# Kernel optimization log

Hardware: AMD Instinct MI355X
Metric: run time of the kernel (lower is better)

Reference implementation:

```python
import jax, jax.numpy as jnp
import numpy as np

T, D, H = 2048, 1024, 16
HS = D // H  # head_size = 64
DFF = 4 * D
LN_EPS = 1e-6


def layernorm(x, scale, bias, eps=LN_EPS):
    mu = jnp.mean(x, axis=-1, keepdims=True)
    var = jnp.mean(jnp.square(x - mu), axis=-1, keepdims=True)
    return (x - mu) * jax.lax.rsqrt(var + eps) * scale + bias


def setup_inputs() -> dict:
    key = jax.random.key(0)
    ks = jax.random.split(key, 12)
    s_in = 1.0 / np.sqrt(D)
    s_ff = 1.0 / np.sqrt(DFF)
    return {
        "x": jax.random.normal(ks[0], (T, D), jnp.float32),
        "Wq": jax.random.normal(ks[1], (H, D, HS), jnp.float32) * s_in,
        "Wk": jax.random.normal(ks[2], (H, D, HS), jnp.float32) * s_in,
        "Wv": jax.random.normal(ks[3], (H, D, HS), jnp.float32) * s_in,
        "Wo": jax.random.normal(ks[4], (D, D), jnp.float32) * s_in,
        "bo": jnp.zeros((D,), jnp.float32),
        "W1": jax.random.normal(ks[5], (D, DFF), jnp.float32) * s_in,
        "b1": jnp.zeros((DFF,), jnp.float32),
        "W2": jax.random.normal(ks[6], (DFF, D), jnp.float32) * s_ff,
        "b2": jnp.zeros((D,), jnp.float32),
        "ln1_scale": jnp.ones((D,), jnp.float32),
        "ln1_bias": jnp.zeros((D,), jnp.float32),
        "ln2_scale": jnp.ones((D,), jnp.float32),
        "ln2_bias": jnp.zeros((D,), jnp.float32),
        "training": 0,
    }


def reference(x, Wq, Wk, Wv, Wo, bo, W1, b1, W2, b2,
              ln1_scale, ln1_bias, ln2_scale, ln2_bias, training):
    # --- pre-LN causal multi-head self-attention ---
    h = layernorm(x, ln1_scale, ln1_bias)
    q = jnp.einsum("td,hdk->htk", h, Wq)  # [H,T,HS]
    k = jnp.einsum("td,hdk->htk", h, Wk)
    v = jnp.einsum("td,hdk->htk", h, Wv)
    scores = jnp.einsum("htk,hsk->hts", q, k) / jnp.sqrt(jnp.float32(HS))
    causal = jnp.tril(jnp.ones((T, T), jnp.float32))
    scores = jnp.where(causal == 0, -jnp.inf, scores)
    wei = jax.nn.softmax(scores, axis=-1)
    av = jnp.einsum("hts,hsk->htk", wei, v)          # [H,T,HS]
    av = av.transpose(1, 0, 2).reshape(T, H * HS)    # concat over heads
    x = x + av @ Wo + bo                              # dropout deterministic -> identity
    # --- pre-LN feed-forward ---
    h2 = layernorm(x, ln2_scale, ln2_bias)
    ff = jax.nn.relu(h2 @ W1 + b1) @ W2 + b2
    x = x + ff
    return x
```

## Files before the change

kernel.cpp:

```cpp
#include <hip/hip_runtime.h>
#include <cstdint>


typedef __bf16 bf16;
typedef __bf16 bf16x4 __attribute__((ext_vector_type(4)));
typedef __bf16 bf16x8 __attribute__((ext_vector_type(8)));
typedef float floatx4 __attribute__((ext_vector_type(4)));

__device__ __forceinline__ void ld_g2l(const bf16* g, bf16* l) {
    __builtin_amdgcn_global_load_lds(
        (const __attribute__((address_space(1))) void*)g,
        (__attribute__((address_space(3))) void*)l, 16, 0, 0);
}

__global__ __launch_bounds__(256) void transpose_cast_kernel(
    const float* __restrict__ src, bf16* __restrict__ dst,
    int R, int C, long long sBatch, long long dBatch)
{
    __shared__ float tile[32][33];
    const int tx = threadIdx.x, ty = threadIdx.y;
    src += (size_t)blockIdx.z * sBatch;
    dst += (size_t)blockIdx.z * dBatch;
    const int c0 = blockIdx.x * 32, r0 = blockIdx.y * 32;
#pragma unroll
    for (int i = ty; i < 32; i += 8)
        tile[i][tx] = src[(size_t)(r0 + i) * C + c0 + tx];
    __syncthreads();
#pragma unroll
    for (int i = ty; i < 32; i += 8)
        dst[(size_t)(c0 + i) * R + r0 + tx] = (bf16)tile[tx][i];
}

__global__ __launch_bounds__(256) void transpose_cast_qkv_kernel(
    const float* __restrict__ Wq, const float* __restrict__ Wk,
    const float* __restrict__ Wv, bf16* __restrict__ dst)
{
    __shared__ float tile[32][33];
    const int tx = threadIdx.x, ty = threadIdx.y;
    const int m = blockIdx.z >> 4, h = blockIdx.z & 15;
    const float* src = (m == 0 ? Wq : (m == 1 ? Wk : Wv)) + h * 65536;
    bf16* d = dst + m * 1048576 + h * 65536;
    const int c0 = blockIdx.x * 32, r0 = blockIdx.y * 32;
#pragma unroll
    for (int i = ty; i < 32; i += 8)
        tile[i][tx] = src[(size_t)(r0 + i) * 64 + c0 + tx];
    __syncthreads();
#pragma unroll
    for (int i = ty; i < 32; i += 8)
        d[(size_t)(c0 + i) * 1024 + r0 + tx] = (bf16)tile[tx][i];
}

__global__ __launch_bounds__(256) void transpose_head_kernel(
    const bf16* __restrict__ qkv, bf16* __restrict__ dst, int colOff)
{
    __shared__ bf16 tile[32][33];
    const int tx = threadIdx.x, ty = threadIdx.y;
    const int h = blockIdx.z;
    const int j0 = blockIdx.x * 32, s0 = blockIdx.y * 32;
#pragma unroll
    for (int i = ty; i < 32; i += 8)
        tile[i][tx] = qkv[(size_t)(s0 + i) * 3072 + colOff + h * 64 + j0 + tx];
    __syncthreads();
#pragma unroll
    for (int i = ty; i < 32; i += 8)
        dst[(size_t)h * 64 * 2048 + (size_t)(j0 + i) * 2048 + s0 + tx] = tile[tx][i];
}

__global__ __launch_bounds__(256) void ln_kernel(
    const float* __restrict__ x, const float* __restrict__ sc,
    const float* __restrict__ bi, bf16* __restrict__ out)
{
    const int row = blockIdx.x;
    const int tid = threadIdx.x;
    const float4 v = ((const float4*)(x + (size_t)row * 1024))[tid];
    float s1 = v.x + v.y + v.z + v.w;
    float s2 = v.x * v.x + v.y * v.y + v.z * v.z + v.w * v.w;
#pragma unroll
    for (int mm = 1; mm < 64; mm <<= 1) {
        s1 += __shfl_xor(s1, mm);
        s2 += __shfl_xor(s2, mm);
    }
    __shared__ float w1[4], w2[4];
    const int wave = tid >> 6, lane = tid & 63;
    if (lane == 0) { w1[wave] = s1; w2[wave] = s2; }
    __syncthreads();
    s1 = w1[0] + w1[1] + w1[2] + w1[3];
    s2 = w2[0] + w2[1] + w2[2] + w2[3];
    const float mu = s1 * (1.f / 1024.f);
    const float var = fmaxf(s2 * (1.f / 1024.f) - mu * mu, 0.f);
    const float rr = rsqrtf(var + 1e-6f);
    const float4 scv = ((const float4*)sc)[tid];
    const float4 biv = ((const float4*)bi)[tid];
    bf16x4 ov;
    ov[0] = (bf16)((v.x - mu) * rr * scv.x + biv.x);
    ov[1] = (bf16)((v.y - mu) * rr * scv.y + biv.y);
    ov[2] = (bf16)((v.z - mu) * rr * scv.z + biv.z);
    ov[3] = (bf16)((v.w - mu) * rr * scv.w + biv.w);
    *(bf16x4*)(out + (size_t)row * 1024 + tid * 4) = ov;
}

__global__ __launch_bounds__(256) void reduce4_kernel(
    const float* __restrict__ p, const float* __restrict__ bias,
    const float* __restrict__ res, float* __restrict__ out)
{
    const int idx = blockIdx.x * 256 + threadIdx.x;
    const int c4 = idx & 255;
    const float4 a0 = ((const float4*)p)[idx];
    const float4 a1 = ((const float4*)(p + 2097152))[idx];
    const float4 a2 = ((const float4*)(p + 4194304))[idx];
    const float4 a3 = ((const float4*)(p + 6291456))[idx];
    const float4 bi = ((const float4*)bias)[c4];
    const float4 r = ((const float4*)res)[idx];
    float4 o;
    o.x = (a0.x + a1.x) + (a2.x + a3.x) + bi.x + r.x;
    o.y = (a0.y + a1.y) + (a2.y + a3.y) + bi.y + r.y;
    o.z = (a0.z + a1.z) + (a2.z + a3.z) + bi.z + r.z;
    o.w = (a0.w + a1.w) + (a2.w + a3.w) + bi.w + r.w;
    ((float4*)out)[idx] = o;
}

template <int MODE, int NG, int MG, int SPLITK>
__global__ __launch_bounds__(256) void gemm128_kernel(
    const bf16* __restrict__ A, const bf16* __restrict__ Bt,
    int N, int K,
    float* __restrict__ outF, bf16* __restrict__ outB,
    const float* __restrict__ bias)
{
    __shared__ __align__(16) bf16 Alds[2][128][32];
    __shared__ __align__(16) bf16 Blds[2][128][32];
    const int tid  = threadIdx.x;
    const int lane = tid & 63;
    const int w    = tid >> 6;
    const int r15  = lane & 15;
    const int quad = lane >> 4;

    const int id    = blockIdx.x + gridDim.x * (blockIdx.y + gridDim.y * blockIdx.z);
    const int xcd   = id & 7;
    const int seq   = id >> 3;
    const int nPerX = gridDim.x / NG;
    const int mPerX = gridDim.y / MG;
    const int nm    = nPerX * mPerX;
    const int z     = seq / nm;
    const int loc   = seq - z * nm;
    const int bn    = ((xcd % NG) * nPerX + (loc % nPerX)) * 128;
    const int bm    = ((xcd / NG) * mPerX + (loc / nPerX)) * 128;

    const int wm = (w >> 1) * 64;
    const int wn = (w & 1) * 64;

    floatx4 acc[4][4];
#pragma unroll
    for (int i = 0; i < 4; ++i)
#pragma unroll
        for (int j = 0; j < 4; ++j) acc[i][j] = (floatx4)(0.f);

    const int KS    = K / SPLITK;
    const int kBase = (SPLITK > 1) ? z * KS : 0;
    const int nIter = KS / 32;

    const int srow = lane >> 2;
    const int gch  = (lane & 3) ^ ((lane >> 3) & 3);
    const bf16* aptr = A + (size_t)(bm + w * 16 + srow) * K + kBase + gch * 8;
    const bf16* bptr = Bt + (size_t)(bn + w * 16 + srow) * K + kBase + gch * 8;

#pragma unroll
    for (int rr = 0; rr < 2; ++rr) {
        ld_g2l(aptr + (size_t)rr * 64 * K, &Alds[0][rr * 64 + w * 16][0]);
        ld_g2l(bptr + (size_t)rr * 64 * K, &Blds[0][rr * 64 + w * 16][0]);
    }

    const int pcs = quad ^ ((r15 >> 1) & 3);

    for (int it = 0; it < nIter; ++it) {
        const int buf = it & 1;
        __syncthreads();
        if (it + 1 < nIter) {
            const int k2 = (it + 1) * 32;
#pragma unroll
            for (int rr = 0; rr < 2; ++rr) {
                ld_g2l(aptr + (size_t)rr * 64 * K + k2, &Alds[buf ^ 1][rr * 64 + w * 16][0]);
                ld_g2l(bptr + (size_t)rr * 64 * K + k2, &Blds[buf ^ 1][rr * 64 + w * 16][0]);
            }
        }
        bf16x8 af[4], bfr[4];
#pragma unroll
        for (int i = 0; i < 4; ++i)
            af[i] = *(const bf16x8*)(&Alds[buf][wm + i * 16 + r15][pcs * 8]);
#pragma unroll
        for (int j = 0; j < 4; ++j)
            bfr[j] = *(const bf16x8*)(&Blds[buf][wn + j * 16 + r15][pcs * 8]);
#pragma unroll
        for (int i = 0; i < 4; ++i)
#pragma unroll
            for (int j = 0; j < 4; ++j)
                acc[i][j] = __builtin_amdgcn_mfma_f32_16x16x32_bf16(
                    af[i], bfr[j], acc[i][j], 0, 0, 0);
    }

    const int row0 = bm + wm + quad * 4;
    const int col0 = bn + wn + r15;
    float* po = (MODE == 3) ? outF + (size_t)z * 2048 * 1024 : outF;
#pragma unroll
    for (int i = 0; i < 4; ++i) {
#pragma unroll
        for (int reg = 0; reg < 4; ++reg) {
            const int row = row0 + i * 16 + reg;
#pragma unroll
            for (int j = 0; j < 4; ++j) {
                const int col = col0 + j * 16;
                float v = acc[i][j][reg];
                if (MODE == 0) {
                    outB[(size_t)row * N + col] = (bf16)v;
                } else if (MODE == 2) {
                    v += bias[col];
                    outB[(size_t)row * N + col] = (bf16)fmaxf(v, 0.f);
                } else {
                    po[(size_t)row * N + col] = v;
                }
            }
        }
    }
}

template <int NG, int MG>
__global__ __launch_bounds__(256) void gemm64_kernel(
    const bf16* __restrict__ A, const bf16* __restrict__ Bt,
    int N, int K,
    float* __restrict__ outF, const float* __restrict__ bias,
    const float* __restrict__ res)
{
    __shared__ __align__(16) bf16 Alds[2][64][64];
    __shared__ __align__(16) bf16 Blds[2][64][64];
    const int tid  = threadIdx.x;
    const int lane = tid & 63;
    const int w    = tid >> 6;
    const int r15  = lane & 15;
    const int quad = lane >> 4;

    const int id    = blockIdx.x + gridDim.x * blockIdx.y;
    const int xcd   = id & 7;
    const int seq   = id >> 3;
    const int nPerX = gridDim.x / NG;
    const int mPerX = gridDim.y / MG;
    const int loc   = seq % (nPerX * mPerX);
    const int bn    = ((xcd % NG) * nPerX + (loc % nPerX)) * 64;
    const int bm    = ((xcd / NG) * mPerX + (loc / nPerX)) * 64;

    const int wm = (w >> 1) * 32;
    const int wn = (w & 1) * 32;

    floatx4 acc[2][2];
#pragma unroll
    for (int i = 0; i < 2; ++i)
#pragma unroll
        for (int j = 0; j < 2; ++j) acc[i][j] = (floatx4)(0.f);

    const int nIter = K / 64;
    const int lrow = lane >> 3;
    const int gch  = (lane & 7) ^ lrow;
    const bf16* aptr = A + (size_t)(bm + w * 16 + lrow) * K + gch * 8;
    const bf16* bptr = Bt + (size_t)(bn + w * 16 + lrow) * K + gch * 8;

#pragma unroll
    for (int t = 0; t < 2; ++t) {
        ld_g2l(aptr + (size_t)t * 8 * K, &Alds[0][w * 16 + t * 8][0]);
        ld_g2l(bptr + (size_t)t * 8 * K, &Blds[0][w * 16 + t * 8][0]);
    }

    for (int it = 0; it < nIter; ++it) {
        const int buf = it & 1;
        __syncthreads();
        if (it + 1 < nIter) {
            const int k2 = (it + 1) * 64;
#pragma unroll
            for (int t = 0; t < 2; ++t) {
                ld_g2l(aptr + (size_t)t * 8 * K + k2, &Alds[buf ^ 1][w * 16 + t * 8][0]);
                ld_g2l(bptr + (size_t)t * 8 * K + k2, &Blds[buf ^ 1][w * 16 + t * 8][0]);
            }
        }
#pragma unroll
        for (int kk = 0; kk < 2; ++kk) {
            const int pc = ((kk * 4 + quad) ^ (r15 & 7)) * 8;
            bf16x8 af[2], bfr[2];
#pragma unroll
            for (int i = 0; i < 2; ++i)
                af[i] = *(const bf16x8*)(&Alds[buf][wm + i * 16 + r15][pc]);
#pragma unroll
            for (int j = 0; j < 2; ++j)
                bfr[j] = *(const bf16x8*)(&Blds[buf][wn + j * 16 + r15][pc]);
#pragma unroll
            for (int i = 0; i < 2; ++i)
#pragma unroll
                for (int j = 0; j < 2; ++j)
                    acc[i][j] = __builtin_amdgcn_mfma_f32_16x16x32_bf16(
                        af[i], bfr[j], acc[i][j], 0, 0, 0);
        }
    }

    const int row0 = bm + wm + quad * 4;
    const int col0 = bn + wn + r15;
#pragma unroll
    for (int i = 0; i < 2; ++i)
#pragma unroll
        for (int reg = 0; reg < 4; ++reg) {
            const int row = row0 + i * 16 + reg;
#pragma unroll
            for (int j = 0; j < 2; ++j) {
                const int col = col0 + j * 16;
                outF[(size_t)row * N + col] =
                    acc[i][j][reg] + bias[col] + res[(size_t)row * N + col];
            }
        }
}

__global__ __launch_bounds__(256) void attn_kernel(
    const bf16* __restrict__ qkv, const bf16* __restrict__ vt,
    bf16* __restrict__ out)
{
    __shared__ __align__(16) bf16 Qs[64][64];
    __shared__ __align__(16) bf16 Ks[2][64][64];
    __shared__ __align__(16) bf16 Vs[2][64][64];
    __shared__ __align__(16) bf16 Ps[4][16][72];

    const int tid  = threadIdx.x;
    const int w    = tid >> 6;
    const int lane = tid & 63;
    const int r15  = lane & 15;
    const int quad = lane >> 4;
    const int rl   = lane >> 3;
    const int gsw  = (lane & 7) ^ (rl & 7);

    const int idp = blockIdx.x + 16 * blockIdx.y;
    const int seq = idp >> 3;
    const int h   = (idp & 7) * 2 + (seq & 1);
    const int qp  = seq >> 1;
    const int qt  = blockIdx.z ? 31 - qp : qp;
    const int qrow0 = qt * 64;

    const bf16* qsec = qkv + h * 64;
    const bf16* ksec = qkv + 1024 + h * 64;
    const bf16* vth  = vt + (size_t)h * 64 * 2048;

#pragma unroll
    for (int t = 0; t < 2; ++t) {
        const int r = t * 32 + w * 8 + rl;
        ld_g2l(qsec + (size_t)(qrow0 + r) * 3072 + gsw * 8, &Qs[t * 32 + w * 8][0]);
        ld_g2l(ksec + (size_t)r * 3072 + gsw * 8, &Ks[0][t * 32 + w * 8][0]);
        ld_g2l(vth + (size_t)r * 2048 + gsw * 8, &Vs[0][t * 32 + w * 8][0]);
    }
    __syncthreads();

    bf16x8 qf[2];
#pragma unroll
    for (int c = 0; c < 2; ++c) {
        const int p = ((c * 4 + quad) ^ (r15 & 7)) * 8;
        qf[c] = *(const bf16x8*)&Qs[w * 16 + r15][p];
    }

    float lacc[4] = {0.f, 0.f, 0.f, 0.f};
    floatx4 O[4];
#pragma unroll
    for (int j = 0; j < 4; ++j) O[j] = (floatx4)(0.f);

#pragma unroll 1
    for (int sb = 0; sb <= qt; ++sb) {
        const int buf = sb & 1;
        if (sb < qt) {
            const int s1 = (sb + 1) * 64;
#pragma unroll
            for (int t = 0; t < 2; ++t) {
                const int r = t * 32 + w * 8 + rl;
                ld_g2l(ksec + (size_t)(s1 + r) * 3072 + gsw * 8, &Ks[buf ^ 1][t * 32 + w * 8][0]);
                ld_g2l(vth + (size_t)r * 2048 + s1 + gsw * 8, &Vs[buf ^ 1][t * 32 + w * 8][0]);
            }
        }

        floatx4 S[4];
#pragma unroll
        for (int j = 0; j < 4; ++j) S[j] = (floatx4)(0.f);
#pragma unroll
        for (int c = 0; c < 2; ++c) {
#pragma unroll
            for (int j = 0; j < 4; ++j) {
                const int p = ((c * 4 + quad) ^ (r15 & 7)) * 8;
                const bf16x8 b = *(const bf16x8*)&Ks[buf][j * 16 + r15][p];
                S[j] = __builtin_amdgcn_mfma_f32_16x16x32_bf16(qf[c], b, S[j], 0, 0, 0);
            }
        }
        const bool diag = (sb == qt);
        const int rowl = w * 16 + quad * 4;
#pragma unroll
        for (int j = 0; j < 4; ++j) {
            const int col = j * 16 + r15;
#pragma unroll
            for (int r = 0; r < 4; ++r) {
                float p = exp2f(fmaf(S[j][r], 0.18033688f, -28.853901f));
                if (diag && col > rowl + r) p = 0.f;
                S[j][r] = p;
                lacc[r] += p;
            }
        }
#pragma unroll
        for (int r = 0; r < 4; ++r)
#pragma unroll
            for (int j = 0; j < 4; ++j)
                Ps[w][quad * 4 + r][j * 16 + r15] = (bf16)S[j][r];
#pragma unroll
        for (int c = 0; c < 2; ++c) {
            const bf16x8 a = *(const bf16x8*)&Ps[w][r15][c * 32 + quad * 8];
#pragma unroll
            for (int j = 0; j < 4; ++j) {
                const int p = ((c * 4 + quad) ^ (r15 & 7)) * 8;
                const bf16x8 b = *(const bf16x8*)&Vs[buf][j * 16 + r15][p];
                O[j] = __builtin_amdgcn_mfma_f32_16x16x32_bf16(a, b, O[j], 0, 0, 0);
            }
        }
        __syncthreads();
    }
#pragma unroll
    for (int r = 0; r < 4; ++r) {
#pragma unroll
        for (int d = 1; d < 16; d <<= 1) lacc[r] += __shfl_xor(lacc[r], d);
    }
#pragma unroll
    for (int r = 0; r < 4; ++r) {
        const float inv = 1.0f / lacc[r];
        const int row = qrow0 + w * 16 + quad * 4 + r;
#pragma unroll
        for (int j = 0; j < 4; ++j)
            out[(size_t)row * 1024 + h * 64 + j * 16 + r15] = (bf16)(O[j][r] * inv);
    }
}

extern "C" void kernel_launch(void* const* d_in, const int* in_sizes, int n_in,
                              void* d_out, int out_size, void* d_ws, size_t ws_size,
                              hipStream_t stream)
{
    const float* x    = (const float*)d_in[0];
    const float* Wq   = (const float*)d_in[1];
    const float* Wk   = (const float*)d_in[2];
    const float* Wv   = (const float*)d_in[3];
    const float* Wo   = (const float*)d_in[4];
    const float* bo   = (const float*)d_in[5];
    const float* W1   = (const float*)d_in[6];
    const float* b1   = (const float*)d_in[7];
    const float* W2   = (const float*)d_in[8];
    const float* b2   = (const float*)d_in[9];
    const float* ln1s = (const float*)d_in[10];
    const float* ln1b = (const float*)d_in[11];
    const float* ln2s = (const float*)d_in[12];
    const float* ln2b = (const float*)d_in[13];

    char* ws = (char*)d_ws;
    bf16*  Wqkvt = (bf16*)(ws + 0);
    bf16*  Wot   = (bf16*)(ws + 6291456);
    bf16*  W1t   = (bf16*)(ws + 8388608);
    bf16*  W2t   = (bf16*)(ws + 16777216);
    bf16*  hbuf  = (bf16*)(ws + 25165824);
    bf16*  QKV   = (bf16*)(ws + 29360128);
    bf16*  Vt    = (bf16*)(ws + 41943040);
    bf16*  Obuf  = (bf16*)(ws + 46137344);
    float* x1    = (float*)(ws + 50331648);
    bf16*  h2    = (bf16*)(ws + 58720256);
    bf16*  ff1   = (bf16*)(ws + 62914560);
    float* psum  = (float*)(ws + 79691776);

    const dim3 tb(32, 8);
    transpose_cast_qkv_kernel<<<dim3(2, 32, 48), tb, 0, stream>>>(Wq, Wk, Wv, Wqkvt);
    transpose_cast_kernel<<<dim3(32, 32, 1), tb, 0, stream>>>(Wo, Wot, 1024, 1024, 0, 0);
    transpose_cast_kernel<<<dim3(128, 32, 1), tb, 0, stream>>>(W1, W1t, 1024, 4096, 0, 0);
    transpose_cast_kernel<<<dim3(32, 128, 1), tb, 0, stream>>>(W2, W2t, 4096, 1024, 0, 0);

    ln_kernel<<<2048, 256, 0, stream>>>(x, ln1s, ln1b, hbuf);
    gemm128_kernel<0,4,2,1><<<dim3(24, 16), 256, 0, stream>>>(hbuf, Wqkvt, 3072, 1024, nullptr, QKV, nullptr);
    transpose_head_kernel<<<dim3(2, 64, 16), tb, 0, stream>>>(QKV, Vt, 2048);
    attn_kernel<<<dim3(16, 16, 2), 256, 0, stream>>>(QKV, Vt, Obuf);
    gemm64_kernel<4,2><<<dim3(16, 32), 256, 0, stream>>>(Obuf, Wot, 1024, 1024, x1, bo, x);
    ln_kernel<<<2048, 256, 0, stream>>>(x1, ln2s, ln2b, h2);
    gemm128_kernel<2,4,2,1><<<dim3(32, 16), 256, 0, stream>>>(h2, W1t, 4096, 1024, nullptr, ff1, b1);
    gemm128_kernel<3,2,4,4><<<dim3(8, 16, 4), 256, 0, stream>>>(ff1, W2t, 1024, 4096, psum, nullptr, nullptr);
    reduce4_kernel<<<2048, 256, 0, stream>>>(psum, b2, x1, (float*)d_out);
}
```

Measured before the change: 278.4 us.

## Merge prep kernels and replace split-K reduce with atomic accumulation into residual

Folds the four weight transpose-casts and the first layernorm into one launch. That layernorm pass also writes x+bo as the initial residual buffer, and the second layernorm writes x1+b2 into the output. The Wo projection and the W2 GEMM now use split-K with fp32 atomicAdd directly into these pre-initialized buffers, which removes the gemm64 kernel, the partial-sum buffer and the reduce kernel. This cuts launch count and partial-sum memory traffic, at the cost of atomic contention and non-deterministic summation order.

New measurement: 295.0 us. 1.06x slower.

```diff
diff --git a/kernel.cpp b/kernel.cpp
--- a/kernel.cpp
+++ b/kernel.cpp
@@ -13,65 +13,12 @@
         (__attribute__((address_space(3))) void*)l, 16, 0, 0);
 }
 
-__global__ __launch_bounds__(256) void transpose_cast_kernel(
-    const float* __restrict__ src, bf16* __restrict__ dst,
-    int R, int C, long long sBatch, long long dBatch)
-{
-    __shared__ float tile[32][33];
-    const int tx = threadIdx.x, ty = threadIdx.y;
-    src += (size_t)blockIdx.z * sBatch;
-    dst += (size_t)blockIdx.z * dBatch;
-    const int c0 = blockIdx.x * 32, r0 = blockIdx.y * 32;
-#pragma unroll
-    for (int i = ty; i < 32; i += 8)
-        tile[i][tx] = src[(size_t)(r0 + i) * C + c0 + tx];
-    __syncthreads();
-#pragma unroll
-    for (int i = ty; i < 32; i += 8)
-        dst[(size_t)(c0 + i) * R + r0 + tx] = (bf16)tile[tx][i];
-}
-
-__global__ __launch_bounds__(256) void transpose_cast_qkv_kernel(
-    const float* __restrict__ Wq, const float* __restrict__ Wk,
-    const float* __restrict__ Wv, bf16* __restrict__ dst)
-{
-    __shared__ float tile[32][33];
-    const int tx = threadIdx.x, ty = threadIdx.y;
-    const int m = blockIdx.z >> 4, h = blockIdx.z & 15;
-    const float* src = (m == 0 ? Wq : (m == 1 ? Wk : Wv)) + h * 65536;
-    bf16* d = dst + m * 1048576 + h * 65536;
-    const int c0 = blockIdx.x * 32, r0 = blockIdx.y * 32;
-#pragma unroll
-    for (int i = ty; i < 32; i += 8)
-        tile[i][tx] = src[(size_t)(r0 + i) * 64 + c0 + tx];
-    __syncthreads();
-#pragma unroll
-    for (int i = ty; i < 32; i += 8)
-        d[(size_t)(c0 + i) * 1024 + r0 + tx] = (bf16)tile[tx][i];
-}
-
-__global__ __launch_bounds__(256) void transpose_head_kernel(
-    const bf16* __restrict__ qkv, bf16* __restrict__ dst, int colOff)
-{
-    __shared__ bf16 tile[32][33];
-    const int tx = threadIdx.x, ty = threadIdx.y;
-    const int h = blockIdx.z;
-    const int j0 = blockIdx.x * 32, s0 = blockIdx.y * 32;
-#pragma unroll
-    for (int i = ty; i < 32; i += 8)
-        tile[i][tx] = qkv[(size_t)(s0 + i) * 3072 + colOff + h * 64 + j0 + tx];
-    __syncthreads();
-#pragma unroll
-    for (int i = ty; i < 32; i += 8)
-        dst[(size_t)h * 64 * 2048 + (size_t)(j0 + i) * 2048 + s0 + tx] = tile[tx][i];
-}
-
-__global__ __launch_bounds__(256) void ln_kernel(
+__device__ __forceinline__ void ln_row_body(
     const float* __restrict__ x, const float* __restrict__ sc,
-    const float* __restrict__ bi, bf16* __restrict__ out)
-{
-    const int row = blockIdx.x;
-    const int tid = threadIdx.x;
+    const float* __restrict__ bi, bf16* __restrict__ out,
+    const float* __restrict__ preBias, float* __restrict__ pre,
+    int row, int tid, float* wred)
+{
     const float4 v = ((const float4*)(x + (size_t)row * 1024))[tid];
     float s1 = v.x + v.y + v.z + v.w;
     float s2 = v.x * v.x + v.y * v.y + v.z * v.z + v.w * v.w;
@@ -80,12 +27,11 @@
         s1 += __shfl_xor(s1, mm);
         s2 += __shfl_xor(s2, mm);
     }
-    __shared__ float w1[4], w2[4];
     const int wave = tid >> 6, lane = tid & 63;
-    if (lane == 0) { w1[wave] = s1; w2[wave] = s2; }
+    if (lane == 0) { wred[wave] = s1; wred[4 + wave] = s2; }
     __syncthreads();
-    s1 = w1[0] + w1[1] + w1[2] + w1[3];
-    s2 = w2[0] + w2[1] + w2[2] + w2[3];
+    s1 = wred[0] + wred[1] + wred[2] + wred[3];
+    s2 = wred[4] + wred[5] + wred[6] + wred[7];
     const float mu = s1 * (1.f / 1024.f);
     const float var = fmaxf(s2 * (1.f / 1024.f) - mu * mu, 0.f);
     const float rr = rsqrtf(var + 1e-6f);
@@ -97,26 +43,85 @@
     ov[2] = (bf16)((v.z - mu) * rr * scv.z + biv.z);
     ov[3] = (bf16)((v.w - mu) * rr * scv.w + biv.w);
     *(bf16x4*)(out + (size_t)row * 1024 + tid * 4) = ov;
-}
-
-__global__ __launch_bounds__(256) void reduce4_kernel(
-    const float* __restrict__ p, const float* __restrict__ bias,
-    const float* __restrict__ res, float* __restrict__ out)
-{
-    const int idx = blockIdx.x * 256 + threadIdx.x;
-    const int c4 = idx & 255;
-    const float4 a0 = ((const float4*)p)[idx];
-    const float4 a1 = ((const float4*)(p + 2097152))[idx];
-    const float4 a2 = ((const float4*)(p + 4194304))[idx];
-    const float4 a3 = ((const float4*)(p + 6291456))[idx];
-    const float4 bi = ((const float4*)bias)[c4];
-    const float4 r = ((const float4*)res)[idx];
-    float4 o;
-    o.x = (a0.x + a1.x) + (a2.x + a3.x) + bi.x + r.x;
-    o.y = (a0.y + a1.y) + (a2.y + a3.y) + bi.y + r.y;
-    o.z = (a0.z + a1.z) + (a2.z + a3.z) + bi.z + r.z;
-    o.w = (a0.w + a1.w) + (a2.w + a3.w) + bi.w + r.w;
-    ((float4*)out)[idx] = o;
+    const float4 pb = ((const float4*)preBias)[tid];
+    float4 po;
+    po.x = v.x + pb.x; po.y = v.y + pb.y; po.z = v.z + pb.z; po.w = v.w + pb.w;
+    ((float4*)(pre + (size_t)row * 1024))[tid] = po;
+}
+
+__global__ __launch_bounds__(256) void prep_kernel(
+    const float* __restrict__ Wq, const float* __restrict__ Wk,
+    const float* __restrict__ Wv, bf16* __restrict__ Wqkvt,
+    const float* __restrict__ Wo, bf16* __restrict__ Wot,
+    const float* __restrict__ W1, bf16* __restrict__ W1t,
+    const float* __restrict__ W2, bf16* __restrict__ W2t,
+    const float* __restrict__ x, const float* __restrict__ ln1s,
+    const float* __restrict__ ln1b, bf16* __restrict__ hbuf,
+    const float* __restrict__ bo, float* __restrict__ x1init)
+{
+    __shared__ float tile[32][33];
+    __shared__ float wred[8];
+    const int b = blockIdx.x;
+    const int tid = threadIdx.x;
+
+    if (b >= 12288) {
+        ln_row_body(x, ln1s, ln1b, hbuf, bo, x1init, b - 12288, tid, wred);
+        return;
+    }
+
+    const int tx = tid & 31, ty = tid >> 5;
+    const float* src; bf16* dst; int R, C, c0, r0;
+    if (b < 3072) {
+        const int bz = b >> 6, by = (b >> 1) & 31, bx = b & 1;
+        const int m = bz >> 4, h = bz & 15;
+        src = (m == 0 ? Wq : (m == 1 ? Wk : Wv)) + h * 65536;
+        dst = Wqkvt + m * 1048576 + h * 65536;
+        R = 1024; C = 64; c0 = bx * 32; r0 = by * 32;
+    } else if (b < 4096) {
+        const int i = b - 3072;
+        src = Wo; dst = Wot; R = 1024; C = 1024;
+        c0 = (i & 31) * 32; r0 = (i >> 5) * 32;
+    } else if (b < 8192) {
+        const int i = b - 4096;
+        src = W1; dst = W1t; R = 1024; C = 4096;
+        c0 = (i & 127) * 32; r0 = (i >> 7) * 32;
+    } else {
+        const int i = b - 8192;
+        src = W2; dst = W2t; R = 4096; C = 1024;
+        c0 = (i & 31) * 32; r0 = (i >> 5) * 32;
+    }
+#pragma unroll
+    for (int i = ty; i < 32; i += 8)
+        tile[i][tx] = src[(size_t)(r0 + i) * C + c0 + tx];
+    __syncthreads();
+#pragma unroll
+    for (int i = ty; i < 32; i += 8)
+        dst[(size_t)(c0 + i) * R + r0 + tx] = (bf16)tile[tx][i];
+}
+
+__global__ __launch_bounds__(256) void ln2_kernel(
+    const float* __restrict__ x, const float* __restrict__ sc,
+    const float* __restrict__ bi, bf16* __restrict__ out,
+    const float* __restrict__ b2, float* __restrict__ dpre)
+{
+    __shared__ float wred[8];
+    ln_row_body(x, sc, bi, out, b2, dpre, blockIdx.x, threadIdx.x, wred);
+}
+
+__global__ __launch_bounds__(256) void transpose_head_kernel(
+    const bf16* __restrict__ qkv, bf16* __restrict__ dst, int colOff)
+{
+    __shared__ bf16 tile[32][33];
+    const int tx = threadIdx.x, ty = threadIdx.y;
+    const int h = blockIdx.z;
+    const int j0 = blockIdx.x * 32, s0 = blockIdx.y * 32;
+#pragma unroll
+    for (int i = ty; i < 32; i += 8)
+        tile[i][tx] = qkv[(size_t)(s0 + i) * 3072 + colOff + h * 64 + j0 + tx];
+    __syncthreads();
+#pragma unroll
+    for (int i = ty; i < 32; i += 8)
+        dst[(size_t)h * 64 * 2048 + (size_t)(j0 + i) * 2048 + s0 + tx] = tile[tx][i];
 }
 
 template <int MODE, int NG, int MG, int SPLITK>
@@ -199,7 +204,6 @@
 
     const int row0 = bm + wm + quad * 4;
     const int col0 = bn + wn + r15;
-    float* po = (MODE == 3) ? outF + (size_t)z * 2048 * 1024 : outF;
 #pragma unroll
     for (int i = 0; i < 4; ++i) {
 #pragma unroll
@@ -215,102 +219,11 @@
                     v += bias[col];
                     outB[(size_t)row * N + col] = (bf16)fmaxf(v, 0.f);
                 } else {
-                    po[(size_t)row * N + col] = v;
+                    atomicAdd(&outF[(size_t)row * N + col], v);
                 }
             }
         }
     }
-}
-
-template <int NG, int MG>
-__global__ __launch_bounds__(256) void gemm64_kernel(
-    const bf16* __restrict__ A, const bf16* __restrict__ Bt,
-    int N, int K,
-    float* __restrict__ outF, const float* __restrict__ bias,
-    const float* __restrict__ res)
-{
-    __shared__ __align__(16) bf16 Alds[2][64][64];
-    __shared__ __align__(16) bf16 Blds[2][64][64];
-    const int tid  = threadIdx.x;
-    const int lane = tid & 63;
-    const int w    = tid >> 6;
-    const int r15  = lane & 15;
-    const int quad = lane >> 4;
-
-    const int id    = blockIdx.x + gridDim.x * blockIdx.y;
-    const int xcd   = id & 7;
-    const int seq   = id >> 3;
-    const int nPerX = gridDim.x / NG;
-    const int mPerX = gridDim.y / MG;
-    const int loc   = seq % (nPerX * mPerX);
-    const int bn    = ((xcd % NG) * nPerX + (loc % nPerX)) * 64;
-    const int bm    = ((xcd / NG) * mPerX + (loc / nPerX)) * 64;
-
-    const int wm = (w >> 1) * 32;
-    const int wn = (w & 1) * 32;
-
-    floatx4 acc[2][2];
-#pragma unroll
-    for (int i = 0; i < 2; ++i)
-#pragma unroll
-        for (int j = 0; j < 2; ++j) acc[i][j] = (floatx4)(0.f);
-
-    const int nIter = K / 64;
-    const int lrow = lane >> 3;
-    const int gch  = (lane & 7) ^ lrow;
-    const bf16* aptr = A + (size_t)(bm + w * 16 + lrow) * K + gch * 8;
-    const bf16* bptr = Bt + (size_t)(bn + w * 16 + lrow) * K + gch * 8;
-
-#pragma unroll
-    for (int t = 0; t < 2; ++t) {
-        ld_g2l(aptr + (size_t)t * 8 * K, &Alds[0][w * 16 + t * 8][0]);
-        ld_g2l(bptr + (size_t)t * 8 * K, &Blds[0][w * 16 + t * 8][0]);
-    }
-
-    for (int it = 0; it < nIter; ++it) {
-        const int buf = it & 1;
-        __syncthreads();
-        if (it + 1 < nIter) {
-            const int k2 = (it + 1) * 64;
-#pragma unroll
-            for (int t = 0; t < 2; ++t) {
-                ld_g2l(aptr + (size_t)t * 8 * K + k2, &Alds[buf ^ 1][w * 16 + t * 8][0]);
-                ld_g2l(bptr + (size_t)t * 8 * K + k2, &Blds[buf ^ 1][w * 16 + t * 8][0]);
-            }
-        }
-#pragma unroll
-        for (int kk = 0; kk < 2; ++kk) {
-            const int pc = ((kk * 4 + quad) ^ (r15 & 7)) * 8;
-            bf16x8 af[2], bfr[2];
-#pragma unroll
-            for (int i = 0; i < 2; ++i)
-                af[i] = *(const bf16x8*)(&Alds[buf][wm + i * 16 + r15][pc]);
-#pragma unroll
-            for (int j = 0; j < 2; ++j)
-                bfr[j] = *(const bf16x8*)(&Blds[buf][wn + j * 16 + r15][pc]);
-#pragma unroll
-            for (int i = 0; i < 2; ++i)
-#pragma unroll
-                for (int j = 0; j < 2; ++j)
-                    acc[i][j] = __builtin_amdgcn_mfma_f32_16x16x32_bf16(
-                        af[i], bfr[j], acc[i][j], 0, 0, 0);
-        }
-    }
-
-    const int row0 = bm + wm + quad * 4;
-    const int col0 = bn + wn + r15;
-#pragma unroll
-    for (int i = 0; i < 2; ++i)
-#pragma unroll
-        for (int reg = 0; reg < 4; ++reg) {
-            const int row = row0 + i * 16 + reg;
-#pragma unroll
-            for (int j = 0; j < 2; ++j) {
-                const int col = col0 + j * 16;
-                outF[(size_t)row * N + col] =
-                    acc[i][j][reg] + bias[col] + res[(size_t)row * N + col];
-            }
-        }
 }
 
 __global__ __launch_bounds__(256) void attn_kernel(
@@ -463,21 +376,17 @@
     float* x1    = (float*)(ws + 50331648);
     bf16*  h2    = (bf16*)(ws + 58720256);
     bf16*  ff1   = (bf16*)(ws + 62914560);
-    float* psum  = (float*)(ws + 79691776);
 
     const dim3 tb(32, 8);
-    transpose_cast_qkv_kernel<<<dim3(2, 32, 48), tb, 0, stream>>>(Wq, Wk, Wv, Wqkvt);
-    transpose_cast_kernel<<<dim3(32, 32, 1), tb, 0, stream>>>(Wo, Wot, 1024, 1024, 0, 0);
-    transpose_cast_kernel<<<dim3(128, 32, 1), tb, 0, stream>>>(W1, W1t, 1024, 4096, 0, 0);
-    transpose_cast_kernel<<<dim3(32, 128, 1), tb, 0, stream>>>(W2, W2t, 4096, 1024, 0, 0);
-
-    ln_kernel<<<2048, 256, 0, stream>>>(x, ln1s, ln1b, hbuf);
+
+    prep_kernel<<<14336, 256, 0, stream>>>(Wq, Wk, Wv, Wqkvt, Wo, Wot,
+                                           W1, W1t, W2, W2t,
+                                           x, ln1s, ln1b, hbuf, bo, x1);
     gemm128_kernel<0,4,2,1><<<dim3(24, 16), 256, 0, stream>>>(hbuf, Wqkvt, 3072, 1024, nullptr, QKV, nullptr);
     transpose_head_kernel<<<dim3(2, 64, 16), tb, 0, stream>>>(QKV, Vt, 2048);
     attn_kernel<<<dim3(16, 16, 2), 256, 0, stream>>>(QKV, Vt, Obuf);
-    gemm64_kernel<4,2><<<dim3(16, 32), 256, 0, stream>>>(Obuf, Wot, 1024, 1024, x1, bo, x);
-    ln_kernel<<<2048, 256, 0, stream>>>(x1, ln2s, ln2b, h2);
+    gemm128_kernel<4,2,4,2><<<dim3(8, 16, 2), 256, 0, stream>>>(Obuf, Wot, 1024, 1024, x1, nullptr, nullptr);
+    ln2_kernel<<<2048, 256, 0, stream>>>(x1, ln2s, ln2b, h2, b2, (float*)d_out);
     gemm128_kernel<2,4,2,1><<<dim3(32, 16), 256, 0, stream>>>(h2, W1t, 4096, 1024, nullptr, ff1, b1);
-    gemm128_kernel<3,2,4,4><<<dim3(8, 16, 4), 256, 0, stream>>>(ff1, W2t, 1024, 4096, psum, nullptr, nullptr);
-    reduce4_kernel<<<2048, 256, 0, stream>>>(psum, b2, x1, (float*)d_out);
-}
+    gemm128_kernel<4,2,4,4><<<dim3(8, 16, 4), 256, 0, stream>>>(ff1, W2t, 1024, 4096, (float*)d_out, nullptr, nullptr);
+}
```
